# Optimization experiments

Measured on AMD Instinct MI355X. Metric: run time of the kernel, lower is better.

Reference implementation:

```python
import jax, jax.numpy as jnp
import numpy as np

N, F, E, B, D = 100000, 256, 128, 8192, 32
K = 16  # ceil(D * threshold 0.5): neighbors kept per relation


def setup_inputs() -> dict:
    key = jax.random.key(0)
    ks = jax.random.split(key, 11)
    s = 0.05
    return {
        "features": jax.random.normal(ks[0], (N, F), jnp.float32),
        "nodes": jax.random.randint(ks[1], (B,), 0, N),
        "n1": jax.random.randint(ks[2], (B, D), 0, N),
        "n2": jax.random.randint(ks[3], (B, D), 0, N),
        "n3": jax.random.randint(ks[4], (B, D), 0, N),
        "wc": jax.random.normal(ks[5], (F, 2), jnp.float32) * s,
        "bc": jnp.zeros((2,), jnp.float32),
        "w1": jax.random.normal(ks[6], (F, E), jnp.float32) * s,
        "w2": jax.random.normal(ks[7], (F, E), jnp.float32) * s,
        "w3": jax.random.normal(ks[8], (F, E), jnp.float32) * s,
        "weight": jax.random.normal(ks[9], (3 * E + F, E), jnp.float32) * s,
    }


def reference(features, nodes, n1, n2, n3, wc, bc, w1, w2, w3, weight):
    # label-aware scores for all nodes (label_clf): [N, 2]
    scores = features @ wc + bc
    s1 = scores[:, 1]                      # label-1 logit used for distance
    center_scores = scores[nodes]          # [B, 2]
    c = s1[nodes]                          # [B]

    def relation(neighs, w_r):
        # label-aware filtering: keep K neighbors with scores closest to center
        dist = jnp.abs(s1[neighs] - c[:, None])          # [B, D]
        _, idx = jax.lax.top_k(-dist, K)                 # smallest distances
        sel = jnp.take_along_axis(neighs, idx, axis=1)   # [B, K]
        mean_feats = jnp.mean(features[sel], axis=1)     # [B, F]
        return jax.nn.relu(mean_feats @ w_r)             # [B, E] intra-agg embed

    r1 = relation(n1, w1)
    r2 = relation(n2, w2)
    r3 = relation(n3, w3)

    self_feats = features[nodes]                          # [B, F]
    cat_feats = jnp.concatenate([self_feats, r1, r2, r3], axis=1)  # [B, F+3E]
    combined = jax.nn.relu(cat_feats @ weight).T          # [E, B]
    return combined, center_scores
```

## Files before the change

kernel.cpp:

```cpp
#include <hip/hip_runtime.h>

#define NN 100000
#define FD 256
#define ED 128
#define BB 8192
#define DD 32
#define KSEL 16

typedef unsigned short ushort_t;

static __device__ __forceinline__ float b2f(ushort_t u) {
    union { float f; unsigned int i; } v; v.i = ((unsigned int)u) << 16; return v.f;
}
static __device__ __forceinline__ ushort_t f2b(float f) {
    union { float f; unsigned int i; } v; v.f = f;
    unsigned int x = v.i;
    x += 0x7fffu + ((x >> 16) & 1u);
    return (ushort_t)(x >> 16);
}
static __device__ __forceinline__ int clampid(int v) {
    return v < 0 ? 0 : (v >= NN ? NN - 1 : v);
}


__global__ __launch_bounds__(256) void k_scores(
    const float* __restrict__ feats, const float* __restrict__ wc,
    const float* __restrict__ bc,
    float* __restrict__ s0a, float* __restrict__ s1a)
{
    const int lane = threadIdx.x & 63;
    const int wave = blockIdx.x * 4 + (threadIdx.x >> 6);
    const int nwaves = gridDim.x * 4;

    const float4 wa  = *(const float4*)(wc + lane * 8);
    const float4 wb_ = *(const float4*)(wc + lane * 8 + 4);
    const float w00 = wa.x, w01 = wa.z, w02 = wb_.x, w03 = wb_.z;
    const float w10 = wa.y, w11 = wa.w, w12 = wb_.y, w13 = wb_.w;
    const float bc0 = bc[0], bc1 = bc[1];

    for (int row = wave; row < NN; row += nwaves) {
        const float4 f4 = *(const float4*)(feats + (size_t)row * FD + lane * 4);
        float s0 = f4.x * w00 + f4.y * w01 + f4.z * w02 + f4.w * w03;
        float s1 = f4.x * w10 + f4.y * w11 + f4.z * w12 + f4.w * w13;
        #pragma unroll
        for (int o = 32; o; o >>= 1) {
            s0 += __shfl_xor(s0, o);
            s1 += __shfl_xor(s1, o);
        }
        if (lane == 0) {
            s0a[row] = s0 + bc0;
            s1a[row] = s1 + bc1;
        }
    }
}

__global__ __launch_bounds__(256) void k_rel(
    const float* __restrict__ feats, const float* __restrict__ s1a,
    const int* __restrict__ nodes,
    const int* __restrict__ n1, const int* __restrict__ n2,
    const int* __restrict__ n3,
    const float* __restrict__ w1, const float* __restrict__ w2,
    const float* __restrict__ w3,
    ushort_t* __restrict__ r_buf)
{
    const int r  = blockIdx.y;
    const int b0 = blockIdx.x * 32;
    const int* nr = (r == 0) ? n1 : (r == 1) ? n2 : n3;
    const float* W = (r == 0) ? w1 : (r == 1) ? w2 : w3;

    __shared__ __align__(16) ushort_t Am[32 * FD];
    __shared__ __align__(16) float Bsm[32 * ED];
    __shared__ int   sl[32 * KSEL];
    __shared__ float cs1[32];
    int* nb = (int*)Bsm;

    const int t    = threadIdx.x;
    const int wv   = t >> 6;
    const int lane = t & 63;

    if (t < 32) cs1[t] = s1a[clampid(nodes[b0 + t])];
    #pragma unroll
    for (int jj = 0; jj < 4; ++jj) {
        const int idx = t + 256 * jj;
        nb[idx] = clampid(nr[(size_t)b0 * DD + idx]);
    }
    __syncthreads();

    #pragma unroll
    for (int jj = 0; jj < 2; ++jj) {
        const int idx = t + 256 * jj;
        sl[idx] = nb[(idx >> 4) * DD + (idx & 15)];
    }
    __syncthreads();

    {
        const int g = t >> 5;
        const int j = t & 31;
        #pragma unroll
        for (int pass = 0; pass < 4; ++pass) {
            const int row = pass * 8 + g;
            const float d = fabsf(s1a[nb[row * DD + j]] - cs1[row]);
            int rank = 0;
            #pragma unroll
            for (int k = 0; k < 32; ++k) {
                const float dk = __shfl(d, k, 32);
                rank += (dk < d) || (dk == d && k < j);
            }
            if (rank < KSEL) sl[row * KSEL + rank] = nb[row * DD + j];
        }
    }
    __syncthreads();

    for (int rr = wv * 8; rr < wv * 8 + 8; rr += 2) {
        float a0 = 0.f, a1 = 0.f, a2 = 0.f, a3 = 0.f;
        float b0v = 0.f, b1v = 0.f, b2v = 0.f, b3v = 0.f;
        #pragma unroll
        for (int k = 0; k < KSEL; ++k) {
            const int s0i = sl[rr * KSEL + k];
            const int s1i = sl[(rr + 1) * KSEL + k];
            const float4 v0 = *(const float4*)(feats + (size_t)s0i * FD + lane * 4);
            const float4 v1 = *(const float4*)(feats + (size_t)s1i * FD + lane * 4);
            a0 += v0.x; a1 += v0.y; a2 += v0.z; a3 += v0.w;
            b0v += v1.x; b1v += v1.y; b2v += v1.z; b3v += v1.w;
        }
        ushort4 oa, ob;
        oa.x = f2b(a0 * 0.0625f);  oa.y = f2b(a1 * 0.0625f);
        oa.z = f2b(a2 * 0.0625f);  oa.w = f2b(a3 * 0.0625f);
        ob.x = f2b(b0v * 0.0625f); ob.y = f2b(b1v * 0.0625f);
        ob.z = f2b(b2v * 0.0625f); ob.w = f2b(b3v * 0.0625f);
        *(ushort4*)(Am + rr * FD + lane * 4)       = oa;
        *(ushort4*)(Am + (rr + 1) * FD + lane * 4) = ob;
    }
    __syncthreads();

    const int bt = (t >> 5) * 4;
    const int et = (t & 31) * 4;
    float acc[4][4] = {};

    for (int k0 = 0; k0 < FD; k0 += 32) {
        #pragma unroll
        for (int jj = 0; jj < 4; ++jj) {
            const int c = t + 256 * jj;
            const int row = c >> 5, col4 = (c & 31) * 4;
            *(float4*)(Bsm + row * ED + col4) =
                *(const float4*)(W + (size_t)(k0 + row) * ED + col4);
        }
        __syncthreads();
        #pragma unroll
        for (int kk = 0; kk < 32; kk += 4) {
            ushort4 av[4];
            #pragma unroll
            for (int i = 0; i < 4; ++i)
                av[i] = *(const ushort4*)(Am + (bt + i) * FD + k0 + kk);
            #pragma unroll
            for (int q = 0; q < 4; ++q) {
                const float4 bv = *(const float4*)(Bsm + (kk + q) * ED + et);
                const float a0 = b2f(q == 0 ? av[0].x : q == 1 ? av[0].y : q == 2 ? av[0].z : av[0].w);
                const float a1 = b2f(q == 0 ? av[1].x : q == 1 ? av[1].y : q == 2 ? av[1].z : av[1].w);
                const float a2 = b2f(q == 0 ? av[2].x : q == 1 ? av[2].y : q == 2 ? av[2].z : av[2].w);
                const float a3 = b2f(q == 0 ? av[3].x : q == 1 ? av[3].y : q == 2 ? av[3].z : av[3].w);
                acc[0][0] += a0 * bv.x; acc[0][1] += a0 * bv.y;
                acc[0][2] += a0 * bv.z; acc[0][3] += a0 * bv.w;
                acc[1][0] += a1 * bv.x; acc[1][1] += a1 * bv.y;
                acc[1][2] += a1 * bv.z; acc[1][3] += a1 * bv.w;
                acc[2][0] += a2 * bv.x; acc[2][1] += a2 * bv.y;
                acc[2][2] += a2 * bv.z; acc[2][3] += a2 * bv.w;
                acc[3][0] += a3 * bv.x; acc[3][1] += a3 * bv.y;
                acc[3][2] += a3 * bv.z; acc[3][3] += a3 * bv.w;
            }
        }
        __syncthreads();
    }

    #pragma unroll
    for (int i = 0; i < 4; ++i) {
        ushort4 o;
        const float v0 = acc[i][0], v1 = acc[i][1], v2 = acc[i][2], v3 = acc[i][3];
        o.x = f2b(v0 > 0.f ? v0 : 0.f);
        o.y = f2b(v1 > 0.f ? v1 : 0.f);
        o.z = f2b(v2 > 0.f ? v2 : 0.f);
        o.w = f2b(v3 > 0.f ? v3 : 0.f);
        *(ushort4*)(r_buf + (size_t)(r * BB + b0 + bt + i) * ED + et) = o;
    }
}

__global__ __launch_bounds__(256) void k_fin(
    const float* __restrict__ feats, const int* __restrict__ nodes,
    const ushort_t* __restrict__ r_buf, const float* __restrict__ weight,
    const float* __restrict__ s0a, const float* __restrict__ s1a,
    float* __restrict__ out)
{
    const int b0 = blockIdx.x * 32;
    const int e0 = blockIdx.y * 64;
    const int t = threadIdx.x;

    __shared__ __align__(16) unsigned char mem[12800];
    float* Asf = (float*)mem;
    float* Bs2 = (float*)(mem + 4608);
    float* Cs  = (float*)mem;
    __shared__ int nid[32];

    if (t < 32) nid[t] = clampid(nodes[b0 + t]);
    __syncthreads();

    if (blockIdx.y == 0 && t < 64) {
        const int i = t >> 1;
        out[(size_t)ED * BB + (size_t)(b0 + i) * 2 + (t & 1)] =
            (t & 1) ? s1a[nid[i]] : s0a[nid[i]];
    }

    const int arow = t >> 3;
    const int acol = (t & 7) * 4;
    const int bt3 = (t >> 4) * 2;
    const int et3 = (t & 15) * 4;
    float acc[2][4] = {};

    for (int k0 = 0; k0 < FD + 3 * ED; k0 += 32) {
        if (k0 < FD) {
            const float4 v = *(const float4*)(feats + (size_t)nid[arow] * FD + k0 + acol);
            Asf[arow * 36 + acol + 0] = v.x;
            Asf[arow * 36 + acol + 1] = v.y;
            Asf[arow * 36 + acol + 2] = v.z;
            Asf[arow * 36 + acol + 3] = v.w;
        } else {
            const int kr = k0 - FD;
            const ushort4 v = *(const ushort4*)(r_buf +
                (size_t)((kr >> 7) * BB + b0 + arow) * ED + (kr & 127) + acol);
            Asf[arow * 36 + acol + 0] = b2f(v.x);
            Asf[arow * 36 + acol + 1] = b2f(v.y);
            Asf[arow * 36 + acol + 2] = b2f(v.z);
            Asf[arow * 36 + acol + 3] = b2f(v.w);
        }
        #pragma unroll
        for (int jj = 0; jj < 2; ++jj) {
            const int c = t + 256 * jj;
            const int row = c >> 4, col4 = (c & 15) * 4;
            *(float4*)(Bs2 + row * 64 + col4) =
                *(const float4*)(weight + (size_t)(k0 + row) * ED + e0 + col4);
        }
        __syncthreads();
        #pragma unroll
        for (int kk = 0; kk < 32; ++kk) {
            const float a0 = Asf[(bt3 + 0) * 36 + kk];
            const float a1 = Asf[(bt3 + 1) * 36 + kk];
            const float4 bv = *(const float4*)(Bs2 + kk * 64 + et3);
            acc[0][0] += a0 * bv.x; acc[0][1] += a0 * bv.y;
            acc[0][2] += a0 * bv.z; acc[0][3] += a0 * bv.w;
            acc[1][0] += a1 * bv.x; acc[1][1] += a1 * bv.y;
            acc[1][2] += a1 * bv.z; acc[1][3] += a1 * bv.w;
        }
        __syncthreads();
    }

    #pragma unroll
    for (int i = 0; i < 2; ++i)
        #pragma unroll
        for (int j = 0; j < 4; ++j) {
            const float v = acc[i][j];
            Cs[(et3 + j) * 36 + bt3 + i] = v > 0.f ? v : 0.f;
        }
    __syncthreads();
    #pragma unroll
    for (int jj = 0; jj < 2; ++jj) {
        const int c = t + 256 * jj;
        const int er = c >> 3;
        const int off = (c & 7) * 4;
        *(float4*)(out + (size_t)(e0 + er) * BB + b0 + off) =
            *(const float4*)(Cs + er * 36 + off);
    }
}

__global__ __launch_bounds__(256) void k_fused(
    const float* __restrict__ feats, const int* __restrict__ nodes,
    const int* __restrict__ n1, const int* __restrict__ n2,
    const int* __restrict__ n3,
    const float* __restrict__ wc, const float* __restrict__ bc,
    const float* __restrict__ w1, const float* __restrict__ w2,
    const float* __restrict__ w3,
    const float* __restrict__ weight, float* __restrict__ out)
{
    __shared__ __align__(16) unsigned char usm[32768];
    __shared__ int      sl[32 * KSEL];
    __shared__ __align__(16) ushort_t Rt[3 * 32 * ED];
    __shared__ int      nid[32];
    __shared__ float    cs1[32];

    int*      nb  = (int*)usm;
    float*    ns1 = (float*)(usm + 4096);
    ushort_t* Am  = (ushort_t*)usm;
    float*    Bsm = (float*)(usm + 16384);
    float*    Asf = (float*)usm;
    float*    Cs  = (float*)usm;

    const int b0   = blockIdx.x * 32;
    const int t    = threadIdx.x;
    const int wv   = t >> 6;
    const int lane = t & 63;

    const float4 wa  = *(const float4*)(wc + lane * 8);
    const float4 wb_ = *(const float4*)(wc + lane * 8 + 4);
    const float w00 = wa.x, w01 = wa.z, w02 = wb_.x, w03 = wb_.z;
    const float w10 = wa.y, w11 = wa.w, w12 = wb_.y, w13 = wb_.w;
    const float bc0 = bc[0], bc1 = bc[1];

    if (t < 32) nid[t] = clampid(nodes[b0 + t]);
    __syncthreads();

    for (int q = 0; q < 8; ++q) {
        const int i = wv * 8 + q;
        const int node = nid[i];
        const float4 f4 = *(const float4*)(feats + (size_t)node * FD + lane * 4);
        float s0 = f4.x * w00 + f4.y * w01 + f4.z * w02 + f4.w * w03;
        float s1 = f4.x * w10 + f4.y * w11 + f4.z * w12 + f4.w * w13;
        #pragma unroll
        for (int o = 32; o; o >>= 1) {
            s0 += __shfl_xor(s0, o);
            s1 += __shfl_xor(s1, o);
        }
        if (lane == 0) {
            cs1[i] = s1 + bc1;
            out[(size_t)ED * BB + (size_t)(b0 + i) * 2]     = s0 + bc0;
            out[(size_t)ED * BB + (size_t)(b0 + i) * 2 + 1] = s1 + bc1;
        }
    }
    __syncthreads();

    const int bt = (t >> 5) * 4;
    const int et = (t & 31) * 4;

    for (int r = 0; r < 3; ++r) {
        const int* nr = (r == 0) ? n1 : (r == 1) ? n2 : n3;
        const float* W = (r == 0) ? w1 : (r == 1) ? w2 : w3;

        #pragma unroll
        for (int jj = 0; jj < 4; ++jj) {
            const int idx = t + 256 * jj;
            nb[idx] = clampid(nr[(size_t)b0 * DD + idx]);
        }
        __syncthreads();

        #pragma unroll
        for (int jj = 0; jj < 2; ++jj) {
            const int idx = t + 256 * jj;
            sl[idx] = nb[(idx >> 4) * DD + (idx & 15)];
        }

        for (int p = wv; p < 32 * DD; p += 4) {
            const int node = nb[p];
            const float4 f4 = *(const float4*)(feats + (size_t)node * FD + lane * 4);
            float s1 = f4.x * w10 + f4.y * w11 + f4.z * w12 + f4.w * w13;
            #pragma unroll
            for (int o = 32; o; o >>= 1) s1 += __shfl_xor(s1, o);
            if (lane == 0) ns1[p] = s1 + bc1;
        }
        __syncthreads();

        {
            const int g = t >> 5;
            const int j = t & 31;
            #pragma unroll
            for (int pass = 0; pass < 4; ++pass) {
                const int row = pass * 8 + g;
                const float d = fabsf(ns1[row * DD + j] - cs1[row]);
                int rank = 0;
                #pragma unroll
                for (int k = 0; k < 32; ++k) {
                    const float dk = __shfl(d, k, 32);
                    rank += (dk < d) || (dk == d && k < j);
                }
                if (rank < KSEL) sl[row * KSEL + rank] = nb[row * DD + j];
            }
        }
        __syncthreads();

        for (int rr = wv * 8; rr < wv * 8 + 8; ++rr) {
            float a0 = 0.f, a1 = 0.f, a2 = 0.f, a3 = 0.f;
            #pragma unroll
            for (int k = 0; k < KSEL; ++k) {
                const int src = sl[rr * KSEL + k];
                const float4 v = *(const float4*)(feats + (size_t)src * FD + lane * 4);
                a0 += v.x; a1 += v.y; a2 += v.z; a3 += v.w;
            }
            ushort4 o;
            o.x = f2b(a0 * 0.0625f); o.y = f2b(a1 * 0.0625f);
            o.z = f2b(a2 * 0.0625f); o.w = f2b(a3 * 0.0625f);
            *(ushort4*)(Am + rr * FD + lane * 4) = o;
        }
        __syncthreads();

        float acc[4][4] = {};
        for (int k0 = 0; k0 < FD; k0 += 32) {
            #pragma unroll
            for (int jj = 0; jj < 4; ++jj) {
                const int c = t + 256 * jj;
                const int row = c >> 5, col4 = (c & 31) * 4;
                *(float4*)(Bsm + row * ED + col4) =
                    *(const float4*)(W + (size_t)(k0 + row) * ED + col4);
            }
            __syncthreads();
            #pragma unroll
            for (int kk = 0; kk < 32; kk += 4) {
                ushort4 av[4];
                #pragma unroll
                for (int i = 0; i < 4; ++i)
                    av[i] = *(const ushort4*)(Am + (bt + i) * FD + k0 + kk);
                #pragma unroll
                for (int q = 0; q < 4; ++q) {
                    const float4 bv = *(const float4*)(Bsm + (kk + q) * ED + et);
                    const float a0 = b2f(q == 0 ? av[0].x : q == 1 ? av[0].y : q == 2 ? av[0].z : av[0].w);
                    const float a1 = b2f(q == 0 ? av[1].x : q == 1 ? av[1].y : q == 2 ? av[1].z : av[1].w);
                    const float a2 = b2f(q == 0 ? av[2].x : q == 1 ? av[2].y : q == 2 ? av[2].z : av[2].w);
                    const float a3 = b2f(q == 0 ? av[3].x : q == 1 ? av[3].y : q == 2 ? av[3].z : av[3].w);
                    acc[0][0] += a0 * bv.x; acc[0][1] += a0 * bv.y;
                    acc[0][2] += a0 * bv.z; acc[0][3] += a0 * bv.w;
                    acc[1][0] += a1 * bv.x; acc[1][1] += a1 * bv.y;
                    acc[1][2] += a1 * bv.z; acc[1][3] += a1 * bv.w;
                    acc[2][0] += a2 * bv.x; acc[2][1] += a2 * bv.y;
                    acc[2][2] += a2 * bv.z; acc[2][3] += a2 * bv.w;
                    acc[3][0] += a3 * bv.x; acc[3][1] += a3 * bv.y;
                    acc[3][2] += a3 * bv.z; acc[3][3] += a3 * bv.w;
                }
            }
            __syncthreads();
        }

        #pragma unroll
        for (int i = 0; i < 4; ++i) {
            ushort4 o;
            const float v0 = acc[i][0], v1 = acc[i][1], v2 = acc[i][2], v3 = acc[i][3];
            o.x = f2b(v0 > 0.f ? v0 : 0.f);
            o.y = f2b(v1 > 0.f ? v1 : 0.f);
            o.z = f2b(v2 > 0.f ? v2 : 0.f);
            o.w = f2b(v3 > 0.f ? v3 : 0.f);
            *(ushort4*)(Rt + (r * 32 + bt + i) * ED + et) = o;
        }
    }

    const int arow = t >> 3;
    const int acol = (t & 7) * 4;
    float acc[4][4] = {};

    for (int k0 = 0; k0 < FD + 3 * ED; k0 += 32) {
        if (k0 < FD) {
            const float4 v = *(const float4*)(feats + (size_t)nid[arow] * FD + k0 + acol);
            Asf[arow * 36 + acol + 0] = v.x;
            Asf[arow * 36 + acol + 1] = v.y;
            Asf[arow * 36 + acol + 2] = v.z;
            Asf[arow * 36 + acol + 3] = v.w;
        } else {
            const int kr = k0 - FD;
            const ushort4 v = *(const ushort4*)(Rt + ((kr >> 7) * 32 + arow) * ED + (kr & 127) + acol);
            Asf[arow * 36 + acol + 0] = b2f(v.x);
            Asf[arow * 36 + acol + 1] = b2f(v.y);
            Asf[arow * 36 + acol + 2] = b2f(v.z);
            Asf[arow * 36 + acol + 3] = b2f(v.w);
        }
        #pragma unroll
        for (int jj = 0; jj < 4; ++jj) {
            const int c = t + 256 * jj;
            const int row = c >> 5, col4 = (c & 31) * 4;
            *(float4*)(Bsm + row * ED + col4) =
                *(const float4*)(weight + (size_t)(k0 + row) * ED + col4);
        }
        __syncthreads();
        #pragma unroll
        for (int kk = 0; kk < 32; ++kk) {
            const float a0 = Asf[(bt + 0) * 36 + kk];
            const float a1 = Asf[(bt + 1) * 36 + kk];
            const float a2 = Asf[(bt + 2) * 36 + kk];
            const float a3 = Asf[(bt + 3) * 36 + kk];
            const float4 bv = *(const float4*)(Bsm + kk * ED + et);
            acc[0][0] += a0 * bv.x; acc[0][1] += a0 * bv.y;
            acc[0][2] += a0 * bv.z; acc[0][3] += a0 * bv.w;
            acc[1][0] += a1 * bv.x; acc[1][1] += a1 * bv.y;
            acc[1][2] += a1 * bv.z; acc[1][3] += a1 * bv.w;
            acc[2][0] += a2 * bv.x; acc[2][1] += a2 * bv.y;
            acc[2][2] += a2 * bv.z; acc[2][3] += a2 * bv.w;
            acc[3][0] += a3 * bv.x; acc[3][1] += a3 * bv.y;
            acc[3][2] += a3 * bv.z; acc[3][3] += a3 * bv.w;
        }
        __syncthreads();
    }

    #pragma unroll
    for (int i = 0; i < 4; ++i)
        #pragma unroll
        for (int j = 0; j < 4; ++j) {
            const float v = acc[i][j];
            Cs[(et + j) * 36 + bt + i] = v > 0.f ? v : 0.f;
        }
    __syncthreads();
    #pragma unroll
    for (int jj = 0; jj < 4; ++jj) {
        const int c = t + 256 * jj;
        const int er = c >> 3;
        const int off = (c & 7) * 4;
        *(float4*)(out + (size_t)er * BB + b0 + off) = *(const float4*)(Cs + er * 36 + off);
    }
}

extern "C" void kernel_launch(void* const* d_in, const int* in_sizes, int n_in,
                              void* d_out, int out_size, void* d_ws, size_t ws_size,
                              hipStream_t stream)
{
    const float* feats  = (const float*)d_in[0];
    const int*   nodes  = (const int*)d_in[1];
    const int*   n1     = (const int*)d_in[2];
    const int*   n2     = (const int*)d_in[3];
    const int*   n3     = (const int*)d_in[4];
    const float* wc     = (const float*)d_in[5];
    const float* bc     = (const float*)d_in[6];
    const float* w1     = (const float*)d_in[7];
    const float* w2     = (const float*)d_in[8];
    const float* w3     = (const float*)d_in[9];
    const float* weight = (const float*)d_in[10];
    float* out = (float*)d_out;

    if (ws_size >= 7091456) {
        char* ws = (char*)d_ws;
        float*    s0a   = (float*)(ws + 0);
        float*    s1a   = (float*)(ws + 400000);
        ushort_t* r_buf = (ushort_t*)(ws + 800000);

        k_scores<<<800, 256, 0, stream>>>(feats, wc, bc, s0a, s1a);
        k_rel<<<dim3(BB / 32, 3), 256, 0, stream>>>(
            feats, s1a, nodes, n1, n2, n3, w1, w2, w3, r_buf);
        k_fin<<<dim3(BB / 32, 2), 256, 0, stream>>>(
            feats, nodes, r_buf, weight, s0a, s1a, out);
    } else {
        k_fused<<<BB / 32, 256, 0, stream>>>(feats, nodes, n1, n2, n3,
                                             wc, bc, w1, w2, w3, weight, out);
    }
}
```

Before: 291.0 us.

## Use bf16 MFMA for final combine GEMM with pre-transposed bf16 weight

Adds a kernel that transposes the combine weight into bf16 [E, 640] layout and a new final kernel that stages self features and relation embeddings as bf16 in LDS and computes the 640x128 projection with 16x16x32 bf16 MFMA instructions. Each block now covers all 128 output columns for 32 batch rows instead of splitting across two blocks, and the ReLU'd result is written out transposed through LDS. This replaces the scalar FP32 FMA GEMM in k_fin. It risks extra precision loss from bf16 rounding of the self features and weights. The new path only runs when the workspace is large enough, otherwise the old kernel is used.

```diff
diff --git a/kernel.cpp b/kernel.cpp
--- a/kernel.cpp
+++ b/kernel.cpp
@@ -8,6 +8,8 @@
 #define KSEL 16
 
 typedef unsigned short ushort_t;
+typedef __attribute__((ext_vector_type(8))) short short8;
+typedef __attribute__((ext_vector_type(4))) float float4v;
 
 static __device__ __forceinline__ float b2f(ushort_t u) {
     union { float f; unsigned int i; } v; v.i = ((unsigned int)u) << 16; return v.f;
@@ -52,6 +54,20 @@
             s1a[row] = s1 + bc1;
         }
     }
+}
+
+__global__ __launch_bounds__(256) void k_wt(
+    const float* __restrict__ weight, ushort_t* __restrict__ wt)
+{
+    const int idx = blockIdx.x * 256 + threadIdx.x;
+    const int n  = idx / 160;
+    const int k4 = (idx % 160) * 4;
+    ushort4 o;
+    o.x = f2b(weight[(size_t)(k4 + 0) * ED + n]);
+    o.y = f2b(weight[(size_t)(k4 + 1) * ED + n]);
+    o.z = f2b(weight[(size_t)(k4 + 2) * ED + n]);
+    o.w = f2b(weight[(size_t)(k4 + 3) * ED + n]);
+    *(ushort4*)(wt + (size_t)n * 640 + k4) = o;
 }
 
 __global__ __launch_bounds__(256) void k_rel(
@@ -181,6 +197,87 @@
         o.z = f2b(v2 > 0.f ? v2 : 0.f);
         o.w = f2b(v3 > 0.f ? v3 : 0.f);
         *(ushort4*)(r_buf + (size_t)(r * BB + b0 + bt + i) * ED + et) = o;
+    }
+}
+
+__global__ __launch_bounds__(256) void k_fin_mfma(
+    const float* __restrict__ feats, const int* __restrict__ nodes,
+    const ushort_t* __restrict__ r_buf, const ushort_t* __restrict__ wt,
+    const float* __restrict__ s0a, const float* __restrict__ s1a,
+    float* __restrict__ out)
+{
+    const int b0 = blockIdx.x * 32;
+    const int t  = threadIdx.x;
+
+    __shared__ __align__(16) ushort_t At[32 * 648];
+    float* Cs = (float*)At;
+    __shared__ int nid[32];
+
+    if (t < 32) nid[t] = clampid(nodes[b0 + t]);
+    __syncthreads();
+
+    if (t < 64) {
+        const int i = t >> 1;
+        out[(size_t)ED * BB + (size_t)(b0 + i) * 2 + (t & 1)] =
+            (t & 1) ? s1a[nid[i]] : s0a[nid[i]];
+    }
+
+    #pragma unroll
+    for (int i = 0; i < 8; ++i) {
+        const int idx = t + 256 * i;
+        const int row = idx >> 6, c4 = idx & 63;
+        const float4 v = *(const float4*)(feats + (size_t)nid[row] * FD + c4 * 4);
+        ushort4 o;
+        o.x = f2b(v.x); o.y = f2b(v.y); o.z = f2b(v.z); o.w = f2b(v.w);
+        *(ushort4*)(At + row * 648 + c4 * 4) = o;
+    }
+    #pragma unroll
+    for (int i = 0; i < 12; ++i) {
+        const int idx = t + 256 * i;
+        const int row = idx / 96;
+        const int c   = (idx % 96) * 4;
+        const ushort4 v = *(const ushort4*)(r_buf +
+            (size_t)((c >> 7) * BB + b0 + row) * ED + (c & 127));
+        *(ushort4*)(At + row * 648 + FD + c) = v;
+    }
+    __syncthreads();
+
+    const int wv   = t >> 6;
+    const int lane = t & 63;
+    const int quad = lane >> 4;
+    const int ln   = lane & 15;
+    const int mt   = wv & 1;
+    const int n0   = (wv >> 1) * 64;
+
+    const ushort_t* Arow  = At + (mt * 16 + ln) * 648 + quad * 8;
+    const ushort_t* Bbase = wt + (size_t)(n0 + ln) * 640 + quad * 8;
+
+    float4v acc[4] = {};
+    for (int k0 = 0; k0 < 640; k0 += 32) {
+        const short8 a = *(const short8*)(Arow + k0);
+        #pragma unroll
+        for (int nt = 0; nt < 4; ++nt) {
+            const short8 b = *(const short8*)(Bbase + nt * 16 * 640 + k0);
+            acc[nt] = __builtin_amdgcn_mfma_f32_16x16x32_bf16(a, b, acc[nt], 0, 0, 0);
+        }
+    }
+    __syncthreads();
+
+    #pragma unroll
+    for (int nt = 0; nt < 4; ++nt)
+        #pragma unroll
+        for (int reg = 0; reg < 4; ++reg) {
+            const float v = acc[nt][reg];
+            const int n = n0 + nt * 16 + ln;
+            const int m = mt * 16 + quad * 4 + reg;
+            Cs[n * 36 + m] = v > 0.f ? v : 0.f;
+        }
+    __syncthreads();
+    #pragma unroll
+    for (int j = 0; j < 4; ++j) {
+        const int idx = t + 256 * j;
+        const int er = idx >> 3, off = (idx & 7) * 4;
+        *(float4*)(out + (size_t)er * BB + b0 + off) = *(const float4*)(Cs + er * 36 + off);
     }
 }
 
@@ -521,12 +618,19 @@
         float*    s0a   = (float*)(ws + 0);
         float*    s1a   = (float*)(ws + 400000);
         ushort_t* r_buf = (ushort_t*)(ws + 800000);
+        ushort_t* wt    = (ushort_t*)(ws + 7091456);
 
         k_scores<<<800, 256, 0, stream>>>(feats, wc, bc, s0a, s1a);
+        if (ws_size >= 7255296)
+            k_wt<<<80, 256, 0, stream>>>(weight, wt);
         k_rel<<<dim3(BB / 32, 3), 256, 0, stream>>>(
             feats, s1a, nodes, n1, n2, n3, w1, w2, w3, r_buf);
-        k_fin<<<dim3(BB / 32, 2), 256, 0, stream>>>(
-            feats, nodes, r_buf, weight, s0a, s1a, out);
+        if (ws_size >= 7255296)
+            k_fin_mfma<<<BB / 32, 256, 0, stream>>>(
+                feats, nodes, r_buf, wt, s0a, s1a, out);
+        else
+            k_fin<<<dim3(BB / 32, 2), 256, 0, stream>>>(
+                feats, nodes, r_buf, weight, s0a, s1a, out);
     } else {
         k_fused<<<BB / 32, 256, 0, stream>>>(feats, nodes, n1, n2, n3,
                                              wc, bc, w1, w2, w3, weight, out);
```

Result: faster. 272.8 us (-6.3%).
